# Kernel optimization log

Measured on AMD Instinct MI355X. Metric: run time of the kernel, lower is better.

## Reference

```python
import jax, jax.numpy as jnp
import numpy as np

V, D, H, F, L, B, T = 32000, 512, 8, 2048, 4, 4, 1024
DK = D // H
S = 0.02  # init scale


def setup_inputs() -> dict:
    key = jax.random.key(0)
    ks = jax.random.split(key, 10)
    inp = {
        'x': jax.random.randint(ks[0], (B, T), 0, V),
        'embed': jax.random.normal(ks[1], (V, D), jnp.float32) * S,
        'Wq': jax.random.normal(ks[2], (L, D, D), jnp.float32) * S,
        'bq': jnp.zeros((L, D), jnp.float32),
        'Wk': jax.random.normal(ks[3], (L, D, D), jnp.float32) * S,
        'bk': jnp.zeros((L, D), jnp.float32),
        'Wv': jax.random.normal(ks[4], (L, D, D), jnp.float32) * S,
        'bv': jnp.zeros((L, D), jnp.float32),
        'Wo': jax.random.normal(ks[5], (L, D, D), jnp.float32) * S,
        'bo': jnp.zeros((L, D), jnp.float32),
        'ln1_s': jnp.ones((L, D), jnp.float32),
        'ln1_b': jnp.zeros((L, D), jnp.float32),
        'W1': jax.random.normal(ks[6], (L, D, F), jnp.float32) * S,
        'b1': jnp.zeros((L, F), jnp.float32),
        'W2': jax.random.normal(ks[7], (L, F, D), jnp.float32) * S,
        'b2': jnp.zeros((L, D), jnp.float32),
        'ln2_s': jnp.ones((L, D), jnp.float32),
        'ln2_b': jnp.zeros((L, D), jnp.float32),
        'lnf_s': jnp.ones((D,), jnp.float32),
        'lnf_b': jnp.zeros((D,), jnp.float32),
        'Wl': jax.random.normal(ks[8], (D, V), jnp.float32) * S,
        'bl': jnp.zeros((V,), jnp.float32),
    }
    return inp


def _layernorm(x, s, b, eps=1e-5):
    m = jnp.mean(x, axis=-1, keepdims=True)
    v = jnp.mean(jnp.square(x - m), axis=-1, keepdims=True)
    return (x - m) * jax.lax.rsqrt(v + eps) * s + b


def _forward(x, embed, Wq, bq, Wk, bk, Wv, bv, Wo, bo, ln1_s, ln1_b,
             W1, b1, W2, b2, ln2_s, ln2_b, lnf_s, lnf_b, Wl, bl):
    Bb, Tt = x.shape
    emb = embed.at[0].set(0.0)  # padding_idx = 0
    h = emb[x]  # [B,T,D]
    # sinusoidal positional encoding
    pos = jnp.arange(Tt, dtype=jnp.float32)[:, None]
    div = jnp.exp(jnp.arange(0, D, 2, dtype=jnp.float32) * (-np.log(10000.0) / D))
    pe = jnp.zeros((Tt, D), jnp.float32)
    pe = pe.at[:, 0::2].set(jnp.sin(pos * div)).at[:, 1::2].set(jnp.cos(pos * div))
    h = h + pe[None]
    # additive causal mask: 0 on/below diag, -inf above
    causal = jnp.triu(jnp.full((Tt, Tt), -jnp.inf, jnp.float32), 1)
    scale = 1.0 / np.sqrt(DK)
    for l in range(L):
        q = (h @ Wq[l] + bq[l]).reshape(Bb, Tt, H, DK)
        k = (h @ Wk[l] + bk[l]).reshape(Bb, Tt, H, DK)
        v = (h @ Wv[l] + bv[l]).reshape(Bb, Tt, H, DK)
        scores = jnp.einsum('bqhd,bkhd->bhqk', q, k) * scale + causal
        attn = jax.nn.softmax(scores, axis=-1)  # dropout=0 -> identity
        o = jnp.einsum('bhqk,bkhd->bqhd', attn, v).reshape(Bb, Tt, D)
        o = o @ Wo[l] + bo[l]
        h = _layernorm(h + o, ln1_s[l], ln1_b[l])
        ff = jax.nn.gelu(h @ W1[l] + b1[l], approximate=False) @ W2[l] + b2[l]
        h = _layernorm(h + ff, ln2_s[l], ln2_b[l])
    h = _layernorm(h, lnf_s, lnf_b)
    return h @ Wl + bl  # [B,T,V] logits


def reference(x, embed, Wq, bq, Wk, bk, Wv, bv, Wo, bo, ln1_s, ln1_b,
              W1, b1, W2, b2, ln2_s, ln2_b, lnf_s, lnf_b, Wl, bl):
    return _forward(x, embed, Wq, bq, Wk, bk, Wv, bv, Wo, bo, ln1_s, ln1_b,
                    W1, b1, W2, b2, ln2_s, ln2_b, lnf_s, lnf_b, Wl, bl)
```

## Files before the change

### kernel.cpp

```cpp
#include <hip/hip_runtime.h>
#include <math.h>

#define Mtot 4096
#define Dd   512
#define Hh   8
#define DKk  64
#define TT   1024
#define Ff   2048
#define Ll   4
#define Vv   32000

typedef __attribute__((ext_vector_type(8))) short bf16x8;
typedef __attribute__((ext_vector_type(4))) float f32x4;
typedef unsigned short u16;

__device__ __forceinline__ u16 f2b(float f) {
    union { float f; unsigned u; } x; x.f = f;
    unsigned r = x.u + 0x7fffu + ((x.u >> 16) & 1u);
    return (u16)(r >> 16);
}

typedef const __attribute__((address_space(1))) unsigned int* gp_t;
typedef __attribute__((address_space(3))) unsigned int* lp_t;
#define GLOAD_LDS16(g, l) __builtin_amdgcn_global_load_lds((gp_t)(const void*)(g), (lp_t)(void*)(l), 16, 0, 0)

#define SWZ(row, c)  ((c) ^ (((row) & 7) << 3))
#define VSWZ(d, c)   ((c) ^ ((((d) ^ ((d) >> 3)) & 7) << 3))

__global__ __launch_bounds__(256) void embed_pe_kernel(const int* __restrict__ x,
                                                       const float* __restrict__ embed,
                                                       float* __restrict__ h,
                                                       u16* __restrict__ hb) {
    int idx = blockIdx.x * 256 + threadIdx.x;
    int d  = idx & (Dd - 1);
    int bt = idx >> 9;
    int t  = bt & (TT - 1);
    int tok = x[bt];
    float val = (tok == 0) ? 0.0f : embed[(size_t)tok * Dd + d];
    int de = d & ~1;
    float ang = (float)t * expf((float)de * (-9.210340371976184f / (float)Dd));
    val += (d & 1) ? cosf(ang) : sinf(ang);
    h[idx] = val;
    hb[idx] = f2b(val);
}

__global__ __launch_bounds__(256) void transpose_all(const float* __restrict__ Wq, const float* __restrict__ Wk,
                                                     const float* __restrict__ Wv, const float* __restrict__ Wo,
                                                     const float* __restrict__ W1, const float* __restrict__ W2,
                                                     const float* __restrict__ Wl,
                                                     u16* __restrict__ WqkvT, u16* __restrict__ WoT,
                                                     u16* __restrict__ W1T, u16* __restrict__ W2T,
                                                     u16* __restrict__ WlT) {
    __shared__ float t[32][33];
    int id = blockIdx.x;
    const float* src; u16* dst; int K, N, tx, ty;
    if (id < 12288) {
        int l = id / 3072, r = id - l * 3072;
        if (r < 768) {
            int which = r >> 8, t2 = r & 255;
            src = (which == 0 ? Wq : which == 1 ? Wk : Wv) + (size_t)l * 262144;
            dst = WqkvT + (size_t)l * 786432 + (size_t)which * 262144;
            K = 512; N = 512; ty = t2 >> 4; tx = t2 & 15;
        } else if (r < 1024) {
            int t2 = r - 768;
            src = Wo + (size_t)l * 262144; dst = WoT + (size_t)l * 262144;
            K = 512; N = 512; ty = t2 >> 4; tx = t2 & 15;
        } else if (r < 2048) {
            int t2 = r - 1024;
            src = W1 + (size_t)l * 1048576; dst = W1T + (size_t)l * 1048576;
            K = 512; N = 2048; ty = t2 >> 6; tx = t2 & 63;
        } else {
            int t2 = r - 2048;
            src = W2 + (size_t)l * 1048576; dst = W2T + (size_t)l * 1048576;
            K = 2048; N = 512; ty = t2 >> 4; tx = t2 & 15;
        }
    } else {
        int t2 = id - 12288;
        src = Wl; dst = WlT; K = 512; N = 32000;
        ty = t2 / 1000; tx = t2 - ty * 1000;
    }
    int n0 = tx * 32, k0 = ty * 32;
    int tid = threadIdx.x, c = tid & 31, rr = tid >> 5;
    #pragma unroll
    for (int i = 0; i < 4; i++)
        t[rr + i * 8][c] = src[(size_t)(k0 + rr + i * 8) * N + n0 + c];
    __syncthreads();
    #pragma unroll
    for (int i = 0; i < 4; i++)
        dst[(size_t)(n0 + rr + i * 8) * K + k0 + c] = f2b(t[c][rr + i * 8]);
}

__global__ __launch_bounds__(256) void biaspack_kernel(const float* __restrict__ bq,
                                                       const float* __restrict__ bk,
                                                       const float* __restrict__ bv,
                                                       float* __restrict__ bqkv) {
    int idx = blockIdx.x * 256 + threadIdx.x;
    int l = idx / 1536, j = idx - l * 1536;
    float v = (j < 512) ? bq[l * 512 + j] : (j < 1024) ? bk[l * 512 + j - 512] : bv[l * 512 + j - 1024];
    bqkv[idx] = v;
}

template<int ACT, int OUTB>
__global__ __launch_bounds__(256) void mfma_gemm(const u16* __restrict__ A,
                                                 const u16* __restrict__ BT,
                                                 const float* __restrict__ bias,
                                                 float* __restrict__ outF,
                                                 u16* __restrict__ outB,
                                                 int M, int N, int K, int gx) {
    __shared__ __align__(16) u16 As[128 * 32];
    __shared__ __align__(16) u16 Bs[128 * 32];
    int nwg = gridDim.x;
    int flat = blockIdx.x;
    int wg = (flat & 7) * (nwg >> 3) + (flat >> 3);
    int bm = wg / gx, bn = wg - bm * gx;
    int tid = threadIdx.x;
    int lane = tid & 63, w = tid >> 6;
    int wr = w >> 1, wc = w & 1;
    int fr = lane & 15, fq = lane >> 4;
    f32x4 acc[4][4] = {};

    const u16* Ab = A + (size_t)(bm * 128 + w * 32 + (lane >> 2)) * K + (lane & 3) * 8;
    const u16* Bb = BT + (size_t)(bn * 128 + w * 32 + (lane >> 2)) * K + (lane & 3) * 8;
    u16* lA0 = &As[(w * 32) * 32];
    u16* lA1 = &As[(w * 32 + 16) * 32];
    u16* lB0 = &Bs[(w * 32) * 32];
    u16* lB1 = &Bs[(w * 32 + 16) * 32];

    for (int k0 = 0; k0 < K; k0 += 32) {
        GLOAD_LDS16(Ab + k0,          lA0);
        GLOAD_LDS16(Ab + 16 * K + k0, lA1);
        GLOAD_LDS16(Bb + k0,          lB0);
        GLOAD_LDS16(Bb + 16 * K + k0, lB1);
        __syncthreads();
        bf16x8 a[4], b[4];
        #pragma unroll
        for (int m = 0; m < 4; m++) a[m] = *(const bf16x8*)&As[(wr * 64 + m * 16 + fr) * 32 + fq * 8];
        #pragma unroll
        for (int n = 0; n < 4; n++) b[n] = *(const bf16x8*)&Bs[(wc * 64 + n * 16 + fr) * 32 + fq * 8];
        __builtin_amdgcn_s_setprio(1);
        #pragma unroll
        for (int m = 0; m < 4; m++)
            #pragma unroll
            for (int n = 0; n < 4; n++)
                acc[m][n] = __builtin_amdgcn_mfma_f32_16x16x32_bf16(a[m], b[n], acc[m][n], 0, 0, 0);
        __builtin_amdgcn_s_setprio(0);
        __syncthreads();
    }

    #pragma unroll
    for (int m = 0; m < 4; m++) {
        #pragma unroll
        for (int n = 0; n < 4; n++) {
            int col = bn * 128 + wc * 64 + n * 16 + fr;
            float bs = bias[col];
            #pragma unroll
            for (int r = 0; r < 4; r++) {
                int row = bm * 128 + wr * 64 + m * 16 + fq * 4 + r;
                float v = acc[m][n][r] + bs;
                if (ACT == 1) v = 0.5f * v * (1.0f + erff(v * 0.7071067811865475f));
                if (OUTB) outB[(size_t)row * N + col] = f2b(v);
                else      outF[(size_t)row * N + col] = v;
            }
        }
    }
}

__global__ __launch_bounds__(256) void attn_mfma(const u16* __restrict__ qkv,
                                                 u16* __restrict__ ob) {
    int qt = (int)gridDim.x - 1 - (int)blockIdx.x;
    int hh = blockIdx.y, b = blockIdx.z;
    __shared__ __align__(16) u16 Qs[64 * 64];
    __shared__ __align__(16) u16 Ks[64 * 64];
    __shared__ __align__(16) u16 Vt[64 * 64];
    __shared__ __align__(16) u16 Ps[4][16 * 64];
    int tid = threadIdx.x;
    int lane = tid & 63, w = tid >> 6;
    int fr = lane & 15, fq = lane >> 4;
    int q0 = qt * 64;

    {
        int r = tid >> 2, c0 = (tid & 3) * 16;
        const u16* src = qkv + ((size_t)(b * TT + q0 + r)) * 1536 + hh * 64 + c0;
        bf16x8 v0 = *(const bf16x8*)src;
        bf16x8 v1 = *(const bf16x8*)(src + 8);
        *(bf16x8*)&Qs[r * 64 + SWZ(r, c0)]     = v0;
        *(bf16x8*)&Qs[r * 64 + SWZ(r, c0 + 8)] = v1;
    }
    __syncthreads();
    bf16x8 aq0 = *(const bf16x8*)&Qs[(w * 16 + fr) * 64 + SWZ(w * 16 + fr, fq * 8)];
    bf16x8 aq1 = *(const bf16x8*)&Qs[(w * 16 + fr) * 64 + SWZ(w * 16 + fr, 32 + fq * 8)];

    f32x4 oa[4] = {};
    float mreg[4], lreg[4];
    #pragma unroll
    for (int i = 0; i < 4; i++) { mreg[i] = -1e30f; lreg[i] = 0.0f; }

    for (int kt = 0; kt <= qt; kt++) {
        __syncthreads();
        {
            int r = tid >> 2, c0 = (tid & 3) * 16;
            const u16* srcK = qkv + ((size_t)(b * TT + kt * 64 + r)) * 1536 + 512 + hh * 64 + c0;
            bf16x8 k0v = *(const bf16x8*)srcK;
            bf16x8 k1v = *(const bf16x8*)(srcK + 8);
            *(bf16x8*)&Ks[r * 64 + SWZ(r, c0)]     = k0v;
            *(bf16x8*)&Ks[r * 64 + SWZ(r, c0 + 8)] = k1v;
            const u16* srcV = srcK + 512;
            bf16x8 vv0 = *(const bf16x8*)srcV;
            bf16x8 vv1 = *(const bf16x8*)(srcV + 8);
            #pragma unroll
            for (int j = 0; j < 8; j++) {
                int d0 = c0 + j, d1 = c0 + 8 + j;
                Vt[d0 * 64 + VSWZ(d0, r)] = (u16)vv0[j];
                Vt[d1 * 64 + VSWZ(d1, r)] = (u16)vv1[j];
            }
        }
        __syncthreads();

        f32x4 sa[4] = {};
        __builtin_amdgcn_s_setprio(1);
        #pragma unroll
        for (int nt = 0; nt < 4; nt++) {
            int krow = nt * 16 + fr;
            bf16x8 b0 = *(const bf16x8*)&Ks[krow * 64 + SWZ(krow, fq * 8)];
            bf16x8 b1 = *(const bf16x8*)&Ks[krow * 64 + SWZ(krow, 32 + fq * 8)];
            sa[nt] = __builtin_amdgcn_mfma_f32_16x16x32_bf16(aq0, b0, sa[nt], 0, 0, 0);
            sa[nt] = __builtin_amdgcn_mfma_f32_16x16x32_bf16(aq1, b1, sa[nt], 0, 0, 0);
        }
        __builtin_amdgcn_s_setprio(0);

        float p[4][4];
        int qg = w * 16 + fq * 4;
        bool diag = (kt == qt);
        #pragma unroll
        for (int nt = 0; nt < 4; nt++)
            #pragma unroll
            for (int i = 0; i < 4; i++) {
                float s = sa[nt][i] * 0.125f;
                if (diag && (nt * 16 + fr > qg + i)) s = -1e30f;
                p[nt][i] = s;
            }

        float mnew[4], fscale[4];
        #pragma unroll
        for (int i = 0; i < 4; i++) {
            float v = fmaxf(fmaxf(p[0][i], p[1][i]), fmaxf(p[2][i], p[3][i]));
            v = fmaxf(v, __shfl_xor(v, 1));
            v = fmaxf(v, __shfl_xor(v, 2));
            v = fmaxf(v, __shfl_xor(v, 4));
            v = fmaxf(v, __shfl_xor(v, 8));
            mnew[i] = fmaxf(mreg[i], v);
            fscale[i] = __expf(mreg[i] - mnew[i]);
            mreg[i] = mnew[i];
        }
        #pragma unroll
        for (int i = 0; i < 4; i++) {
            float sum = 0.f;
            #pragma unroll
            for (int nt = 0; nt < 4; nt++) {
                float e = __expf(p[nt][i] - mnew[i]);
                p[nt][i] = e;
                sum += e;
            }
            sum += __shfl_xor(sum, 1);
            sum += __shfl_xor(sum, 2);
            sum += __shfl_xor(sum, 4);
            sum += __shfl_xor(sum, 8);
            lreg[i] = lreg[i] * fscale[i] + sum;
        }
        #pragma unroll
        for (int nn = 0; nn < 4; nn++)
            #pragma unroll
            for (int i = 0; i < 4; i++)
                oa[nn][i] *= fscale[i];

        u16* ps = &Ps[w][0];
        #pragma unroll
        for (int nt = 0; nt < 4; nt++)
            #pragma unroll
            for (int i = 0; i < 4; i++) {
                int row = fq * 4 + i, col = nt * 16 + fr;
                ps[row * 64 + SWZ(row, col)] = f2b(p[nt][i]);
            }
        bf16x8 pa0 = *(const bf16x8*)&ps[fr * 64 + SWZ(fr, fq * 8)];
        bf16x8 pa1 = *(const bf16x8*)&ps[fr * 64 + SWZ(fr, 32 + fq * 8)];
        __builtin_amdgcn_s_setprio(1);
        #pragma unroll
        for (int nn = 0; nn < 4; nn++) {
            int drow = nn * 16 + fr;
            bf16x8 vb0 = *(const bf16x8*)&Vt[drow * 64 + VSWZ(drow, fq * 8)];
            bf16x8 vb1 = *(const bf16x8*)&Vt[drow * 64 + VSWZ(drow, 32 + fq * 8)];
            oa[nn] = __builtin_amdgcn_mfma_f32_16x16x32_bf16(pa0, vb0, oa[nn], 0, 0, 0);
            oa[nn] = __builtin_amdgcn_mfma_f32_16x16x32_bf16(pa1, vb1, oa[nn], 0, 0, 0);
        }
        __builtin_amdgcn_s_setprio(0);
    }

    #pragma unroll
    for (int i = 0; i < 4; i++) {
        float inv = 1.0f / lreg[i];
        size_t row = (size_t)(b * TT + q0 + w * 16 + fq * 4 + i) * Dd + hh * 64;
        #pragma unroll
        for (int nn = 0; nn < 4; nn++)
            ob[row + nn * 16 + fr] = f2b(oa[nn][i] * inv);
    }
}

__global__ __launch_bounds__(256) void ln_kernel(float* __restrict__ h,
                                                 const float* __restrict__ delta,
                                                 const float* __restrict__ gs,
                                                 const float* __restrict__ gb,
                                                 u16* __restrict__ hb) {
    __shared__ float red[256];
    int row = blockIdx.x, tid = threadIdx.x;
    size_t base = (size_t)row * Dd;
    float x0 = h[base + tid], x1 = h[base + tid + 256];
    if (delta != nullptr) { x0 += delta[base + tid]; x1 += delta[base + tid + 256]; }
    red[tid] = x0 + x1; __syncthreads();
    for (int st = 128; st > 0; st >>= 1) { if (tid < st) red[tid] += red[tid + st]; __syncthreads(); }
    float m = red[0] * (1.0f / Dd); __syncthreads();
    float d0 = x0 - m, d1 = x1 - m;
    red[tid] = d0 * d0 + d1 * d1; __syncthreads();
    for (int st = 128; st > 0; st >>= 1) { if (tid < st) red[tid] += red[tid + st]; __syncthreads(); }
    float r = rsqrtf(red[0] * (1.0f / Dd) + 1e-5f);
    float y0 = d0 * r * gs[tid] + gb[tid];
    float y1 = d1 * r * gs[tid + 256] + gb[tid + 256];
    h[base + tid] = y0;         h[base + tid + 256] = y1;
    hb[base + tid] = f2b(y0);   hb[base + tid + 256] = f2b(y1);
}

extern "C" void kernel_launch(void* const* d_in, const int* in_sizes, int n_in,
                              void* d_out, int out_size, void* d_ws, size_t ws_size,
                              hipStream_t stream) {
    const int*   x     = (const int*)  d_in[0];
    const float* embed = (const float*)d_in[1];
    const float* Wq    = (const float*)d_in[2];
    const float* bq    = (const float*)d_in[3];
    const float* Wk    = (const float*)d_in[4];
    const float* bk    = (const float*)d_in[5];
    const float* Wv    = (const float*)d_in[6];
    const float* bv    = (const float*)d_in[7];
    const float* Wo    = (const float*)d_in[8];
    const float* bo    = (const float*)d_in[9];
    const float* ln1_s = (const float*)d_in[10];
    const float* ln1_b = (const float*)d_in[11];
    const float* W1    = (const float*)d_in[12];
    const float* b1    = (const float*)d_in[13];
    const float* W2    = (const float*)d_in[14];
    const float* b2    = (const float*)d_in[15];
    const float* ln2_s = (const float*)d_in[16];
    const float* ln2_b = (const float*)d_in[17];
    const float* lnf_s = (const float*)d_in[18];
    const float* lnf_b = (const float*)d_in[19];
    const float* Wl    = (const float*)d_in[20];
    const float* bl    = (const float*)d_in[21];

    char* wp = (char*)d_ws;
    float* h    = (float*)wp;  wp += (size_t)Mtot * Dd * 4;
    float* pb   = (float*)wp;  wp += (size_t)Mtot * Dd * 4;
    u16*   hb   = (u16*)wp;    wp += (size_t)Mtot * Dd * 2;
    u16*   qkvb = (u16*)wp;    wp += (size_t)Mtot * 1536 * 2;
    u16*   obb  = (u16*)wp;    wp += (size_t)Mtot * Dd * 2;
    u16*   fbb  = (u16*)wp;    wp += (size_t)Mtot * Ff * 2;
    u16*   WlT  = (u16*)wp;    wp += (size_t)Vv * Dd * 2;
    float* bqkv = (float*)wp;  wp += (size_t)Ll * 1536 * 4;

    char* op = (char*)d_out;
    u16* WqkvT = (u16*)op;  op += (size_t)Ll * 1536 * Dd * 2;
    u16* WoT   = (u16*)op;  op += (size_t)Ll * Dd * Dd * 2;
    u16* W1T   = (u16*)op;  op += (size_t)Ll * Ff * Dd * 2;
    u16* W2T   = (u16*)op;  op += (size_t)Ll * Dd * Ff * 2;

    transpose_all<<<28288, 256, 0, stream>>>(Wq, Wk, Wv, Wo, W1, W2, Wl, WqkvT, WoT, W1T, W2T, WlT);
    biaspack_kernel<<<24, 256, 0, stream>>>(bq, bk, bv, bqkv);
    embed_pe_kernel<<<(Mtot * Dd) / 256, 256, 0, stream>>>(x, embed, h, hb);

    for (int l = 0; l < Ll; l++) {
        mfma_gemm<0, 1><<<(1536 / 128) * (Mtot / 128), 256, 0, stream>>>(
            hb, WqkvT + (size_t)l * 1536 * Dd, bqkv + l * 1536, nullptr, qkvb, Mtot, 1536, Dd, 1536 / 128);
        attn_mfma<<<dim3(TT / 64, Hh, 4), 256, 0, stream>>>(qkvb, obb);
        mfma_gemm<0, 0><<<(Dd / 128) * (Mtot / 128), 256, 0, stream>>>(
            obb, WoT + (size_t)l * Dd * Dd, bo + l * Dd, pb, nullptr, Mtot, Dd, Dd, Dd / 128);
        ln_kernel<<<Mtot, 256, 0, stream>>>(h, pb, ln1_s + l * Dd, ln1_b + l * Dd, hb);
        mfma_gemm<1, 1><<<(Ff / 128) * (Mtot / 128), 256, 0, stream>>>(
            hb, W1T + (size_t)l * Ff * Dd, b1 + l * Ff, nullptr, fbb, Mtot, Ff, Dd, Ff / 128);
        mfma_gemm<0, 0><<<(Dd / 128) * (Mtot / 128), 256, 0, stream>>>(
            fbb, W2T + (size_t)l * Dd * Ff, b2 + l * Dd, pb, nullptr, Mtot, Dd, Ff, Dd / 128);
        ln_kernel<<<Mtot, 256, 0, stream>>>(h, pb, ln2_s + l * Dd, ln2_b + l * Dd, hb);
    }

    ln_kernel<<<Mtot, 256, 0, stream>>>(h, nullptr, lnf_s, lnf_b, hb);
    mfma_gemm<0, 0><<<(Vv / 128) * (Mtot / 128), 256, 0, stream>>>(
        hb, WlT, bl, (float*)d_out, nullptr, Mtot, Vv, Dd, Vv / 128);
}
```

Baseline: 898.1 us.

## Double-buffer GEMM with 512 threads, split-K narrow GEMMs, wave-per-row layernorm

The GEMM now uses 8 waves per block and double-buffered LDS, so the next K tile is prefetched while MFMAs run on the current one, with one barrier per iteration. The narrow Wo and W2 GEMMs (N=512) are split into two K halves written to separate buffers, which doubles the block count. The layernorm kernel adds both partial sums and now handles one row per wavefront with shuffle reductions and vectorized loads and stores. The cost is an extra fp32 partial buffer and an extra launch per split, plus higher register pressure under launch_bounds(512,4).

```diff
diff --git a/kernel.cpp b/kernel.cpp
--- a/kernel.cpp
+++ b/kernel.cpp
@@ -23,6 +23,7 @@
 typedef const __attribute__((address_space(1))) unsigned int* gp_t;
 typedef __attribute__((address_space(3))) unsigned int* lp_t;
 #define GLOAD_LDS16(g, l) __builtin_amdgcn_global_load_lds((gp_t)(const void*)(g), (lp_t)(void*)(l), 16, 0, 0)
+#define VMCNT0 asm volatile("s_waitcnt vmcnt(0)" ::: "memory")
 
 #define SWZ(row, c)  ((c) ^ (((row) & 7) << 3))
 #define VSWZ(d, c)   ((c) ^ ((((d) ^ ((d) >> 3)) & 7) << 3))
@@ -101,58 +102,64 @@
 }
 
 template<int ACT, int OUTB>
-__global__ __launch_bounds__(256) void mfma_gemm(const u16* __restrict__ A,
-                                                 const u16* __restrict__ BT,
-                                                 const float* __restrict__ bias,
-                                                 float* __restrict__ outF,
-                                                 u16* __restrict__ outB,
-                                                 int M, int N, int K, int gx) {
-    __shared__ __align__(16) u16 As[128 * 32];
-    __shared__ __align__(16) u16 Bs[128 * 32];
-    int nwg = gridDim.x;
-    int flat = blockIdx.x;
+__global__ __launch_bounds__(512, 4) void mfma_gemm(const u16* __restrict__ A,
+                                                    const u16* __restrict__ BT,
+                                                    const float* __restrict__ bias,
+                                                    float* __restrict__ outF,
+                                                    u16* __restrict__ outB,
+                                                    int M, int N, int K, int kbase, int klen, int gx) {
+    __shared__ __align__(16) u16 As[2][128 * 32];
+    __shared__ __align__(16) u16 Bs[2][128 * 32];
+    int tid = threadIdx.x;
+    int lane = tid & 63, w = tid >> 6;
+    int nwg = gridDim.x, flat = blockIdx.x;
     int wg = (flat & 7) * (nwg >> 3) + (flat >> 3);
     int bm = wg / gx, bn = wg - bm * gx;
-    int tid = threadIdx.x;
-    int lane = tid & 63, w = tid >> 6;
-    int wr = w >> 1, wc = w & 1;
+    int wr = w >> 2, wc = w & 3;
     int fr = lane & 15, fq = lane >> 4;
-    f32x4 acc[4][4] = {};
-
-    const u16* Ab = A + (size_t)(bm * 128 + w * 32 + (lane >> 2)) * K + (lane & 3) * 8;
-    const u16* Bb = BT + (size_t)(bn * 128 + w * 32 + (lane >> 2)) * K + (lane & 3) * 8;
-    u16* lA0 = &As[(w * 32) * 32];
-    u16* lA1 = &As[(w * 32 + 16) * 32];
-    u16* lB0 = &Bs[(w * 32) * 32];
-    u16* lB1 = &Bs[(w * 32 + 16) * 32];
-
-    for (int k0 = 0; k0 < K; k0 += 32) {
-        GLOAD_LDS16(Ab + k0,          lA0);
-        GLOAD_LDS16(Ab + 16 * K + k0, lA1);
-        GLOAD_LDS16(Bb + k0,          lB0);
-        GLOAD_LDS16(Bb + 16 * K + k0, lB1);
-        __syncthreads();
-        bf16x8 a[4], b[4];
-        #pragma unroll
-        for (int m = 0; m < 4; m++) a[m] = *(const bf16x8*)&As[(wr * 64 + m * 16 + fr) * 32 + fq * 8];
-        #pragma unroll
-        for (int n = 0; n < 4; n++) b[n] = *(const bf16x8*)&Bs[(wc * 64 + n * 16 + fr) * 32 + fq * 8];
+
+    int srow = tid >> 2, scol = (tid & 3) * 8;
+    const u16* Ab = A  + (size_t)(bm * 128 + srow) * K + kbase + scol;
+    const u16* Bb = BT + (size_t)(bn * 128 + srow) * K + kbase + scol;
+
+    f32x4 acc[4][2] = {};
+    int nk = klen >> 5;
+
+    GLOAD_LDS16(Ab, &As[0][w * 512]);
+    GLOAD_LDS16(Bb, &Bs[0][w * 512]);
+    VMCNT0;
+    __builtin_amdgcn_s_barrier();
+
+    int cur = 0;
+    for (int kt = 0; kt < nk; kt++) {
+        if (kt + 1 < nk) {
+            GLOAD_LDS16(Ab + (kt + 1) * 32, &As[cur ^ 1][w * 512]);
+            GLOAD_LDS16(Bb + (kt + 1) * 32, &Bs[cur ^ 1][w * 512]);
+        }
+        bf16x8 a[4], b[2];
+        #pragma unroll
+        for (int m = 0; m < 4; m++) a[m] = *(const bf16x8*)&As[cur][(wr * 64 + m * 16 + fr) * 32 + fq * 8];
+        #pragma unroll
+        for (int n = 0; n < 2; n++) b[n] = *(const bf16x8*)&Bs[cur][(wc * 32 + n * 16 + fr) * 32 + fq * 8];
         __builtin_amdgcn_s_setprio(1);
         #pragma unroll
         for (int m = 0; m < 4; m++)
             #pragma unroll
-            for (int n = 0; n < 4; n++)
+            for (int n = 0; n < 2; n++)
                 acc[m][n] = __builtin_amdgcn_mfma_f32_16x16x32_bf16(a[m], b[n], acc[m][n], 0, 0, 0);
         __builtin_amdgcn_s_setprio(0);
-        __syncthreads();
+        __builtin_amdgcn_sched_barrier(0);
+        VMCNT0;
+        __builtin_amdgcn_s_barrier();
+        cur ^= 1;
     }
 
     #pragma unroll
     for (int m = 0; m < 4; m++) {
         #pragma unroll
-        for (int n = 0; n < 4; n++) {
-            int col = bn * 128 + wc * 64 + n * 16 + fr;
-            float bs = bias[col];
+        for (int n = 0; n < 2; n++) {
+            int col = bn * 128 + wc * 32 + n * 16 + fr;
+            float bs = bias ? bias[col] : 0.0f;
             #pragma unroll
             for (int r = 0; r < 4; r++) {
                 int row = bm * 128 + wr * 64 + m * 16 + fq * 4 + r;
@@ -306,26 +313,42 @@
 }
 
 __global__ __launch_bounds__(256) void ln_kernel(float* __restrict__ h,
-                                                 const float* __restrict__ delta,
+                                                 const float* __restrict__ d1,
+                                                 const float* __restrict__ d2,
                                                  const float* __restrict__ gs,
                                                  const float* __restrict__ gb,
                                                  u16* __restrict__ hb) {
-    __shared__ float red[256];
-    int row = blockIdx.x, tid = threadIdx.x;
-    size_t base = (size_t)row * Dd;
-    float x0 = h[base + tid], x1 = h[base + tid + 256];
-    if (delta != nullptr) { x0 += delta[base + tid]; x1 += delta[base + tid + 256]; }
-    red[tid] = x0 + x1; __syncthreads();
-    for (int st = 128; st > 0; st >>= 1) { if (tid < st) red[tid] += red[tid + st]; __syncthreads(); }
-    float m = red[0] * (1.0f / Dd); __syncthreads();
-    float d0 = x0 - m, d1 = x1 - m;
-    red[tid] = d0 * d0 + d1 * d1; __syncthreads();
-    for (int st = 128; st > 0; st >>= 1) { if (tid < st) red[tid] += red[tid + st]; __syncthreads(); }
-    float r = rsqrtf(red[0] * (1.0f / Dd) + 1e-5f);
-    float y0 = d0 * r * gs[tid] + gb[tid];
-    float y1 = d1 * r * gs[tid + 256] + gb[tid + 256];
-    h[base + tid] = y0;         h[base + tid + 256] = y1;
-    hb[base + tid] = f2b(y0);   hb[base + tid + 256] = f2b(y1);
+    int w = threadIdx.x >> 6, lane = threadIdx.x & 63;
+    int row = (blockIdx.x << 2) + w;
+    size_t base = (size_t)row * Dd + lane * 8;
+    f32x4 v0 = *(const f32x4*)&h[base];
+    f32x4 v1 = *(const f32x4*)&h[base + 4];
+    if (d1) { v0 += *(const f32x4*)&d1[base]; v1 += *(const f32x4*)&d1[base + 4]; }
+    if (d2) { v0 += *(const f32x4*)&d2[base]; v1 += *(const f32x4*)&d2[base + 4]; }
+    float s = v0[0] + v0[1] + v0[2] + v0[3] + v1[0] + v1[1] + v1[2] + v1[3];
+    #pragma unroll
+    for (int st = 1; st < 64; st <<= 1) s += __shfl_xor(s, st);
+    float m = s * (1.0f / Dd);
+    float q = 0.f;
+    #pragma unroll
+    for (int j = 0; j < 4; j++) { float a = v0[j] - m, b = v1[j] - m; q += a * a + b * b; }
+    #pragma unroll
+    for (int st = 1; st < 64; st <<= 1) q += __shfl_xor(q, st);
+    float r = rsqrtf(q * (1.0f / Dd) + 1e-5f);
+    f32x4 g0 = *(const f32x4*)&gs[lane * 8],     g1 = *(const f32x4*)&gs[lane * 8 + 4];
+    f32x4 c0 = *(const f32x4*)&gb[lane * 8],     c1 = *(const f32x4*)&gb[lane * 8 + 4];
+    f32x4 y0, y1;
+    bf16x8 yb;
+    #pragma unroll
+    for (int j = 0; j < 4; j++) {
+        y0[j] = (v0[j] - m) * r * g0[j] + c0[j];
+        y1[j] = (v1[j] - m) * r * g1[j] + c1[j];
+        yb[j]     = (short)f2b(y0[j]);
+        yb[j + 4] = (short)f2b(y1[j]);
+    }
+    *(f32x4*)&h[base]     = y0;
+    *(f32x4*)&h[base + 4] = y1;
+    *(bf16x8*)&hb[base]   = yb;
 }
 
 extern "C" void kernel_launch(void* const* d_in, const int* in_sizes, int n_in,
@@ -357,6 +380,7 @@
     char* wp = (char*)d_ws;
     float* h    = (float*)wp;  wp += (size_t)Mtot * Dd * 4;
     float* pb   = (float*)wp;  wp += (size_t)Mtot * Dd * 4;
+    float* pb2  = (float*)wp;  wp += (size_t)Mtot * Dd * 4;
     u16*   hb   = (u16*)wp;    wp += (size_t)Mtot * Dd * 2;
     u16*   qkvb = (u16*)wp;    wp += (size_t)Mtot * 1536 * 2;
     u16*   obb  = (u16*)wp;    wp += (size_t)Mtot * Dd * 2;
@@ -375,20 +399,30 @@
     embed_pe_kernel<<<(Mtot * Dd) / 256, 256, 0, stream>>>(x, embed, h, hb);
 
     for (int l = 0; l < Ll; l++) {
-        mfma_gemm<0, 1><<<(1536 / 128) * (Mtot / 128), 256, 0, stream>>>(
-            hb, WqkvT + (size_t)l * 1536 * Dd, bqkv + l * 1536, nullptr, qkvb, Mtot, 1536, Dd, 1536 / 128);
+        mfma_gemm<0, 1><<<(1536 / 128) * (Mtot / 128), 512, 0, stream>>>(
+            hb, WqkvT + (size_t)l * 1536 * Dd, bqkv + l * 1536, nullptr, qkvb,
+            Mtot, 1536, Dd, 0, Dd, 1536 / 128);
         attn_mfma<<<dim3(TT / 64, Hh, 4), 256, 0, stream>>>(qkvb, obb);
-        mfma_gemm<0, 0><<<(Dd / 128) * (Mtot / 128), 256, 0, stream>>>(
-            obb, WoT + (size_t)l * Dd * Dd, bo + l * Dd, pb, nullptr, Mtot, Dd, Dd, Dd / 128);
-        ln_kernel<<<Mtot, 256, 0, stream>>>(h, pb, ln1_s + l * Dd, ln1_b + l * Dd, hb);
-        mfma_gemm<1, 1><<<(Ff / 128) * (Mtot / 128), 256, 0, stream>>>(
-            hb, W1T + (size_t)l * Ff * Dd, b1 + l * Ff, nullptr, fbb, Mtot, Ff, Dd, Ff / 128);
-        mfma_gemm<0, 0><<<(Dd / 128) * (Mtot / 128), 256, 0, stream>>>(
-            fbb, W2T + (size_t)l * Dd * Ff, b2 + l * Dd, pb, nullptr, Mtot, Dd, Ff, Dd / 128);
-        ln_kernel<<<Mtot, 256, 0, stream>>>(h, pb, ln2_s + l * Dd, ln2_b + l * Dd, hb);
-    }
-
-    ln_kernel<<<Mtot, 256, 0, stream>>>(h, nullptr, lnf_s, lnf_b, hb);
-    mfma_gemm<0, 0><<<(Vv / 128) * (Mtot / 128), 256, 0, stream>>>(
-        hb, WlT, bl, (float*)d_out, nullptr, Mtot, Vv, Dd, Vv / 128);
-}
+        mfma_gemm<0, 0><<<(Dd / 128) * (Mtot / 128), 512, 0, stream>>>(
+            obb, WoT + (size_t)l * Dd * Dd, bo + l * Dd, pb, nullptr,
+            Mtot, Dd, Dd, 0, Dd / 2, Dd / 128);
+        mfma_gemm<0, 0><<<(Dd / 128) * (Mtot / 128), 512, 0, stream>>>(
+            obb, WoT + (size_t)l * Dd * Dd, nullptr, pb2, nullptr,
+            Mtot, Dd, Dd, Dd / 2, Dd / 2, Dd / 128);
+        ln_kernel<<<Mtot / 4, 256, 0, stream>>>(h, pb, pb2, ln1_s + l * Dd, ln1_b + l * Dd, hb);
+        mfma_gemm<1, 1><<<(Ff / 128) * (Mtot / 128), 512, 0, stream>>>(
+            hb, W1T + (size_t)l * Ff * Dd, b1 + l * Ff, nullptr, fbb,
+            Mtot, Ff, Dd, 0, Dd, Ff / 128);
+        mfma_gemm<0, 0><<<(Dd / 128) * (Mtot / 128), 512, 0, stream>>>(
+            fbb, W2T + (size_t)l * Dd * Ff, b2 + l * Dd, pb, nullptr,
+            Mtot, Dd, Ff, 0, Ff / 2, Dd / 128);
+        mfma_gemm<0, 0><<<(Dd / 128) * (Mtot / 128), 512, 0, stream>>>(
+            fbb, W2T + (size_t)l * Dd * Ff, nullptr, pb2, nullptr,
+            Mtot, Dd, Ff, Ff / 2, Ff / 2, Dd / 128);
+        ln_kernel<<<Mtot / 4, 256, 0, stream>>>(h, pb, pb2, ln2_s + l * Dd, ln2_b + l * Dd, hb);
+    }
+
+    ln_kernel<<<Mtot / 4, 256, 0, stream>>>(h, nullptr, nullptr, lnf_s, lnf_b, hb);
+    mfma_gemm<0, 0><<<(Vv / 128) * (Mtot / 128), 512, 0, stream>>>(
+        hb, WlT, bl, (float*)d_out, nullptr, Mtot, Vv, Dd, 0, Dd, Vv / 128);
+}
```

Measured after the change: 903.1 us. About the same (+0.6%).
